# Kernel optimization log

Hardware: AMD Instinct MI355X
Metric: run time of the kernel (lower is better)

## Reference

```python
import jax, jax.numpy as jnp
import numpy as np

N_NODES = 60000
IN_CH = 128
HID = 32
ACT_DIM = 6
N_EDGES = 600000


def setup_inputs() -> dict:
    key = jax.random.key(0)
    ks = jax.random.split(key, 10)
    state = jax.random.normal(ks[0], (N_NODES, IN_CH), dtype=jnp.float32)
    edge_index = jax.random.randint(ks[1], (2, N_EDGES), 0, N_NODES, dtype=jnp.int64)
    s_g = 1.0 / np.sqrt(IN_CH)
    s_h = 1.0 / np.sqrt(HID)
    Wg = jax.random.uniform(ks[2], (IN_CH, IN_CH), jnp.float32, -s_g, s_g)
    bg = jax.random.uniform(ks[3], (IN_CH,), jnp.float32, -s_g, s_g)
    W1 = jax.random.uniform(ks[4], (IN_CH, HID), jnp.float32, -s_g, s_g)
    b1 = jax.random.uniform(ks[5], (HID,), jnp.float32, -s_g, s_g)
    W2 = jax.random.uniform(ks[6], (HID, HID), jnp.float32, -s_h, s_h)
    b2 = jax.random.uniform(ks[7], (HID,), jnp.float32, -s_h, s_h)
    W3 = jax.random.uniform(ks[8], (HID, 1), jnp.float32, -s_h, s_h)
    b3 = jax.random.uniform(ks[9], (1,), jnp.float32, -s_h, s_h)
    return {"state": state, "Wg": Wg, "bg": bg, "W1": W1, "b1": b1,
            "W2": W2, "b2": b2, "W3": W3, "b3": b3, "edge_index": edge_index}


def reference(state, Wg, bg, W1, b1, W2, b2, W3, b3, edge_index):
    N = state.shape[0]
    # GCNConv: add self-loops, symmetric degree normalization
    loop = jnp.arange(N, dtype=edge_index.dtype)
    src = jnp.concatenate([edge_index[0], loop])
    dst = jnp.concatenate([edge_index[1], loop])
    deg = jax.ops.segment_sum(jnp.ones_like(dst, dtype=state.dtype), dst, num_segments=N)
    dinv = jax.lax.rsqrt(deg)  # deg >= 1 thanks to self-loops
    norm = dinv[src] * dinv[dst]  # [E+N]
    h = state @ Wg  # [N, C]
    agg = jax.ops.segment_sum(h[src] * norm[:, None], dst, num_segments=N) + bg
    out = jax.nn.relu(agg)
    x = (out + state).reshape(-1, ACT_DIM, IN_CH)  # [B, 6, C]
    x = jax.nn.leaky_relu(x @ W1 + b1)
    x = jax.nn.leaky_relu(x @ W2 + b2)
    conc = jax.nn.softplus(x @ W3 + b3)[..., 0]  # [B, 6]
    # deterministic, mode==0
    action = conc / (conc.sum() + 1e-20)
    return action
```

## Files before the change

### kernel.cpp

```cpp
#include <hip/hip_runtime.h>
#include <hip/hip_bf16.h>
#include <math.h>

#define N_NODES 60000
#define IN_CH   128
#define HID     32
#define N_EDGES 600000
#define CAP     48

#define WS_CNT    0
#define WS_SUM    60000
#define WS_BUCKET 60008
#define WS_HS     2940032
#define WS_X      10620032

typedef float  v4f __attribute__((ext_vector_type(4)));
typedef short  v8s __attribute__((ext_vector_type(8)));

static __device__ inline short f2bf(float f) {
    __hip_bfloat16 h = __float2bfloat16(f);
    union { __hip_bfloat16 h; short s; } u; u.h = h; return u.s;
}

__global__ void k_hist(const int* __restrict__ eidx, int* __restrict__ cnt,
                       int* __restrict__ bucket) {
    int i = blockIdx.x * blockDim.x + threadIdx.x;
    if (i >= N_EDGES) return;
    int s = eidx[i];
    int d = eidx[N_EDGES + i];
    int slot = atomicAdd(&cnt[d], 1);
    if (slot < CAP) bucket[d * CAP + slot] = s;
}

__launch_bounds__(256)
__global__ void k_gemm(const float* __restrict__ state, const float* __restrict__ Wg,
                       const int* __restrict__ cnt, unsigned short* __restrict__ hs) {
    __shared__ __align__(16) short Bs[128 * 136];
    const int t = threadIdx.x;
    for (int idx = t; idx < 128 * 128; idx += 256) {
        int k = idx >> 7, n = idx & 127;
        Bs[n * 136 + k] = f2bf(Wg[idx]);
    }
    __syncthreads();

    const int w = t >> 6, lane = t & 63;
    const int quad = lane >> 4, m = lane & 15;
    const int rowBase = blockIdx.x * 64;
    int arow = rowBase + w * 16 + m;
    if (arow > N_NODES - 1) arow = N_NODES - 1;

    v8s a[4];
    const float4* sp = (const float4*)(state + (size_t)arow * 128);
#pragma unroll
    for (int q = 0; q < 4; ++q) {
        float4 v0 = sp[q * 8 + quad * 2];
        float4 v1 = sp[q * 8 + quad * 2 + 1];
        v8s af;
        af[0] = f2bf(v0.x); af[1] = f2bf(v0.y); af[2] = f2bf(v0.z); af[3] = f2bf(v0.w);
        af[4] = f2bf(v1.x); af[5] = f2bf(v1.y); af[6] = f2bf(v1.z); af[7] = f2bf(v1.w);
        a[q] = af;
    }

    v4f acc[8];
#pragma unroll
    for (int tt = 0; tt < 8; ++tt) acc[tt] = (v4f)0.f;

#pragma unroll
    for (int tt = 0; tt < 8; ++tt) {
        const short* bp = &Bs[(tt * 16 + m) * 136];
#pragma unroll
        for (int q = 0; q < 4; ++q) {
            v8s b = *(const v8s*)(bp + q * 32 + quad * 8);
            acc[tt] = __builtin_amdgcn_mfma_f32_16x16x32_bf16(a[q], b, acc[tt], 0, 0, 0);
        }
    }

    float dinv[4];
#pragma unroll
    for (int r = 0; r < 4; ++r) {
        int rr = rowBase + w * 16 + quad * 4 + r;
        dinv[r] = (rr < N_NODES) ? rsqrtf((float)cnt[rr] + 1.0f) : 0.f;
    }
#pragma unroll
    for (int tt = 0; tt < 8; ++tt) {
#pragma unroll
        for (int r = 0; r < 4; ++r) {
            int rr = rowBase + w * 16 + quad * 4 + r;
            if (rr < N_NODES)
                hs[(size_t)rr * 128 + tt * 16 + m] = (unsigned short)f2bf(acc[tt][r] * dinv[r]);
        }
    }
}

__launch_bounds__(256)
__global__ void k_gather(const unsigned short* __restrict__ hs, const float* __restrict__ state,
                         const int* __restrict__ cnt, const int* __restrict__ bucket,
                         const float* __restrict__ bg, float* __restrict__ x) {
    const int wave = threadIdx.x >> 6, lane = threadIdx.x & 63;
    const int row = blockIdx.x * 4 + wave;
    if (row >= N_NODES) return;
    const int ci = cnt[row];
    const float dinv = rsqrtf((float)ci + 1.0f);
    const int nb = ci < CAP ? ci : CAP;

    int slot = (lane < nb) ? bucket[row * CAP + lane] : 0;

    const unsigned int* hp = (const unsigned int*)hs;
    float ax, ay;
    {
        unsigned int u = hp[row * 64 + lane];
        ax = __uint_as_float(u << 16);
        ay = __uint_as_float(u & 0xffff0000u);
    }
    int s = 0;
    for (; s + 8 <= nb; s += 8) {
        unsigned int u0 = hp[__shfl(slot, s + 0, 64) * 64 + lane];
        unsigned int u1 = hp[__shfl(slot, s + 1, 64) * 64 + lane];
        unsigned int u2 = hp[__shfl(slot, s + 2, 64) * 64 + lane];
        unsigned int u3 = hp[__shfl(slot, s + 3, 64) * 64 + lane];
        unsigned int u4 = hp[__shfl(slot, s + 4, 64) * 64 + lane];
        unsigned int u5 = hp[__shfl(slot, s + 5, 64) * 64 + lane];
        unsigned int u6 = hp[__shfl(slot, s + 6, 64) * 64 + lane];
        unsigned int u7 = hp[__shfl(slot, s + 7, 64) * 64 + lane];
        ax += __uint_as_float(u0 << 16) + __uint_as_float(u1 << 16)
            + __uint_as_float(u2 << 16) + __uint_as_float(u3 << 16)
            + __uint_as_float(u4 << 16) + __uint_as_float(u5 << 16)
            + __uint_as_float(u6 << 16) + __uint_as_float(u7 << 16);
        ay += __uint_as_float(u0 & 0xffff0000u) + __uint_as_float(u1 & 0xffff0000u)
            + __uint_as_float(u2 & 0xffff0000u) + __uint_as_float(u3 & 0xffff0000u)
            + __uint_as_float(u4 & 0xffff0000u) + __uint_as_float(u5 & 0xffff0000u)
            + __uint_as_float(u6 & 0xffff0000u) + __uint_as_float(u7 & 0xffff0000u);
    }
    for (; s + 4 <= nb; s += 4) {
        unsigned int u0 = hp[__shfl(slot, s + 0, 64) * 64 + lane];
        unsigned int u1 = hp[__shfl(slot, s + 1, 64) * 64 + lane];
        unsigned int u2 = hp[__shfl(slot, s + 2, 64) * 64 + lane];
        unsigned int u3 = hp[__shfl(slot, s + 3, 64) * 64 + lane];
        ax += __uint_as_float(u0 << 16) + __uint_as_float(u1 << 16)
            + __uint_as_float(u2 << 16) + __uint_as_float(u3 << 16);
        ay += __uint_as_float(u0 & 0xffff0000u) + __uint_as_float(u1 & 0xffff0000u)
            + __uint_as_float(u2 & 0xffff0000u) + __uint_as_float(u3 & 0xffff0000u);
    }
    for (; s < nb; ++s) {
        unsigned int u = hp[__shfl(slot, s, 64) * 64 + lane];
        ax += __uint_as_float(u << 16);
        ay += __uint_as_float(u & 0xffff0000u);
    }
    float2 bgv = ((const float2*)bg)[lane];
    float2 st  = ((const float2*)state)[row * 64 + lane];
    float2 o;
    o.x = fmaxf(fmaf(dinv, ax, bgv.x), 0.f) + st.x;
    o.y = fmaxf(fmaf(dinv, ay, bgv.y), 0.f) + st.y;
    ((float2*)x)[row * 64 + lane] = o;
}

__launch_bounds__(256)
__global__ void k_mlp(const float* __restrict__ x,
                      const float* __restrict__ W1, const float* __restrict__ b1,
                      const float* __restrict__ W2, const float* __restrict__ b2,
                      const float* __restrict__ W3, const float* __restrict__ b3,
                      float* __restrict__ out, float* __restrict__ sum) {
    __shared__ float4 W1s[128 * 8];
    __shared__ float4 W2s[32 * 8];
    __shared__ float  W3s[32];
    __shared__ float  wred[4];
    const int t = threadIdx.x;
#pragma unroll
    for (int i = 0; i < 4; ++i) W1s[t + 256 * i] = ((const float4*)W1)[t + 256 * i];
    W2s[t] = ((const float4*)W2)[t];
    if (t < 32) W3s[t] = W3[t];
    __syncthreads();

    const int r = blockIdx.x * 256 + t;
    float sp = 0.f;
    if (r < N_NODES) {
        float h1[32];
#pragma unroll
        for (int j = 0; j < 32; ++j) h1[j] = b1[j];
        const float4* xr = (const float4*)(x + (size_t)r * 128);
#pragma unroll 4
        for (int k4 = 0; k4 < 32; ++k4) {
            float4 xv = xr[k4];
            float xa[4] = {xv.x, xv.y, xv.z, xv.w};
#pragma unroll
            for (int kk = 0; kk < 4; ++kk) {
                float xk = xa[kk];
#pragma unroll
                for (int j4 = 0; j4 < 8; ++j4) {
                    float4 w = W1s[(k4 * 4 + kk) * 8 + j4];
                    h1[j4 * 4 + 0] = fmaf(xk, w.x, h1[j4 * 4 + 0]);
                    h1[j4 * 4 + 1] = fmaf(xk, w.y, h1[j4 * 4 + 1]);
                    h1[j4 * 4 + 2] = fmaf(xk, w.z, h1[j4 * 4 + 2]);
                    h1[j4 * 4 + 3] = fmaf(xk, w.w, h1[j4 * 4 + 3]);
                }
            }
        }
        float z1[32];
#pragma unroll
        for (int j = 0; j < 32; ++j) z1[j] = h1[j] > 0.f ? h1[j] : 0.01f * h1[j];
        float h2[32];
#pragma unroll
        for (int j = 0; j < 32; ++j) h2[j] = b2[j];
#pragma unroll
        for (int k = 0; k < 32; ++k) {
            float zk = z1[k];
#pragma unroll
            for (int j4 = 0; j4 < 8; ++j4) {
                float4 w = W2s[k * 8 + j4];
                h2[j4 * 4 + 0] = fmaf(zk, w.x, h2[j4 * 4 + 0]);
                h2[j4 * 4 + 1] = fmaf(zk, w.y, h2[j4 * 4 + 1]);
                h2[j4 * 4 + 2] = fmaf(zk, w.z, h2[j4 * 4 + 2]);
                h2[j4 * 4 + 3] = fmaf(zk, w.w, h2[j4 * 4 + 3]);
            }
        }
        float a3 = b3[0];
#pragma unroll
        for (int j = 0; j < 32; ++j) {
            float z2 = h2[j] > 0.f ? h2[j] : 0.01f * h2[j];
            a3 = fmaf(z2, W3s[j], a3);
        }
        sp = fmaxf(a3, 0.f) + log1pf(expf(-fabsf(a3)));
        out[r] = sp;
    }
    float p = sp;
#pragma unroll
    for (int off = 32; off >= 1; off >>= 1) p += __shfl_xor(p, off, 64);
    if ((t & 63) == 0) wred[t >> 6] = p;
    __syncthreads();
    if (t == 0) atomicAdd(sum, (wred[0] + wred[1]) + (wred[2] + wred[3]));
}

__global__ void k_norm(const float* __restrict__ sum, float* __restrict__ out) {
    int i = blockIdx.x * blockDim.x + threadIdx.x;
    if (i < N_NODES) out[i] = out[i] / (*sum + 1e-20f);
}

extern "C" void kernel_launch(void* const* d_in, const int* in_sizes, int n_in,
                              void* d_out, int out_size, void* d_ws, size_t ws_size,
                              hipStream_t stream) {
    const float* state = (const float*)d_in[0];
    const float* Wg    = (const float*)d_in[1];
    const float* bg    = (const float*)d_in[2];
    const float* W1    = (const float*)d_in[3];
    const float* b1    = (const float*)d_in[4];
    const float* W2    = (const float*)d_in[5];
    const float* b2    = (const float*)d_in[6];
    const float* W3    = (const float*)d_in[7];
    const float* b3    = (const float*)d_in[8];
    const int*   eidx  = (const int*)d_in[9];
    float* out = (float*)d_out;

    int*   wi = (int*)d_ws;
    float* wf = (float*)d_ws;
    int*   cnt    = wi + WS_CNT;
    float* sum    = wf + WS_SUM;
    int*   bucket = wi + WS_BUCKET;
    unsigned short* hs = (unsigned short*)(wf + WS_HS);
    float* x      = wf + WS_X;

    hipMemsetAsync(cnt, 0, 60001 * sizeof(int), stream);
    k_hist<<<(N_EDGES + 255) / 256, 256, 0, stream>>>(eidx, cnt, bucket);
    k_gemm<<<(N_NODES + 63) / 64, 256, 0, stream>>>(state, Wg, cnt, hs);
    k_gather<<<(N_NODES + 3) / 4, 256, 0, stream>>>(hs, state, cnt, bucket, bg, x);
    k_mlp<<<(N_NODES + 255) / 256, 256, 0, stream>>>(x, W1, b1, W2, b2, W3, b3, out, sum);
    k_norm<<<(N_NODES + 255) / 256, 256, 0, stream>>>(sum, out);
}
```

Before: 190.4 us.

## Fuse gather and MLP into persistent kernel, pre-convert Wg, shrink bucket to u16

Merges the neighbor gather and the per-node MLP into one persistent grid-stride kernel. Each wave computes a node's aggregated features into shared memory and evaluates the small MLP cooperatively with lane-parallel dot products and shuffles, so the fp32 x intermediate is never written to or read from global memory. Wg is converted to transposed bf16 once in the histogram kernel rather than in every GEMM block, and bucket indices are stored as 16-bit values. Node ids up to 60000 fit in an unsigned short, but the MLP now runs per row with heavy shuffle and LDS traffic, which may reduce throughput.

After: 240.1 us. 1.26x slower.

```diff
diff --git a/kernel.cpp b/kernel.cpp
--- a/kernel.cpp
+++ b/kernel.cpp
@@ -10,9 +10,9 @@
 
 #define WS_CNT    0
 #define WS_SUM    60000
-#define WS_BUCKET 60008
-#define WS_HS     2940032
-#define WS_X      10620032
+#define WS_WGT    60004
+#define WS_BUCKET 68200
+#define WS_HS     1508200
 
 typedef float  v4f __attribute__((ext_vector_type(4)));
 typedef short  v8s __attribute__((ext_vector_type(8)));
@@ -23,23 +23,30 @@
 }
 
 __global__ void k_hist(const int* __restrict__ eidx, int* __restrict__ cnt,
-                       int* __restrict__ bucket) {
+                       unsigned short* __restrict__ bucket,
+                       const float* __restrict__ Wg, unsigned short* __restrict__ wgt) {
     int i = blockIdx.x * blockDim.x + threadIdx.x;
-    if (i >= N_EDGES) return;
-    int s = eidx[i];
-    int d = eidx[N_EDGES + i];
-    int slot = atomicAdd(&cnt[d], 1);
-    if (slot < CAP) bucket[d * CAP + slot] = s;
+    if (i < N_EDGES) {
+        int s = eidx[i];
+        int d = eidx[N_EDGES + i];
+        int slot = atomicAdd(&cnt[d], 1);
+        if (slot < CAP) bucket[d * CAP + slot] = (unsigned short)s;
+    }
+    if (i < IN_CH * IN_CH) {
+        int k = i >> 7, n = i & 127;
+        wgt[n * 128 + k] = (unsigned short)f2bf(Wg[i]);
+    }
 }
 
 __launch_bounds__(256)
-__global__ void k_gemm(const float* __restrict__ state, const float* __restrict__ Wg,
+__global__ void k_gemm(const float* __restrict__ state, const unsigned short* __restrict__ wgt,
                        const int* __restrict__ cnt, unsigned short* __restrict__ hs) {
     __shared__ __align__(16) short Bs[128 * 136];
     const int t = threadIdx.x;
-    for (int idx = t; idx < 128 * 128; idx += 256) {
-        int k = idx >> 7, n = idx & 127;
-        Bs[n * 136 + k] = f2bf(Wg[idx]);
+    for (int i = t; i < 2048; i += 256) {
+        int n = i >> 4, kc = i & 15;
+        v8s v = *(const v8s*)(wgt + n * 128 + kc * 8);
+        *(v8s*)&Bs[n * 136 + kc * 8] = v;
     }
     __syncthreads();
 
@@ -64,7 +71,6 @@
     v4f acc[8];
 #pragma unroll
     for (int tt = 0; tt < 8; ++tt) acc[tt] = (v4f)0.f;
-
 #pragma unroll
     for (int tt = 0; tt < 8; ++tt) {
         const short* bp = &Bs[(tt * 16 + m) * 136];
@@ -93,139 +99,112 @@
 }
 
 __launch_bounds__(256)
-__global__ void k_gather(const unsigned short* __restrict__ hs, const float* __restrict__ state,
-                         const int* __restrict__ cnt, const int* __restrict__ bucket,
-                         const float* __restrict__ bg, float* __restrict__ x) {
-    const int wave = threadIdx.x >> 6, lane = threadIdx.x & 63;
-    const int row = blockIdx.x * 4 + wave;
-    if (row >= N_NODES) return;
-    const int ci = cnt[row];
-    const float dinv = rsqrtf((float)ci + 1.0f);
-    const int nb = ci < CAP ? ci : CAP;
-
-    int slot = (lane < nb) ? bucket[row * CAP + lane] : 0;
-
+__global__ void k_gather_mlp(const unsigned short* __restrict__ hs, const float* __restrict__ state,
+                             const int* __restrict__ cnt, const unsigned short* __restrict__ bucket,
+                             const float* __restrict__ bg,
+                             const float* __restrict__ W1, const float* __restrict__ b1,
+                             const float* __restrict__ W2, const float* __restrict__ b2,
+                             const float* __restrict__ W3, const float* __restrict__ b3,
+                             float* __restrict__ out, float* __restrict__ sum) {
+    __shared__ float W1s[128 * 32];
+    __shared__ float W2s[32 * 32];
+    __shared__ float xs[4][128];
+    __shared__ float wred[4];
+    const int t = threadIdx.x;
+#pragma unroll
+    for (int i = 0; i < 4; ++i)
+        ((float4*)W1s)[t + 256 * i] = ((const float4*)W1)[t + 256 * i];
+    ((float4*)W2s)[t] = ((const float4*)W2)[t];
+    __syncthreads();
+
+    const int wave = t >> 6, lane = t & 63;
+    const int j = lane & 31;
+    const int khalf = (lane >> 5) * 64;
+    const int k2 = (lane >> 5) * 16;
+    const float2 bgv = ((const float2*)bg)[lane];
+    const float b1r = b1[j];
+    const float b2r = b2[j];
+    const float w3r = (lane < 32) ? W3[j] : 0.f;
+    const float b3v = b3[0];
     const unsigned int* hp = (const unsigned int*)hs;
-    float ax, ay;
-    {
-        unsigned int u = hp[row * 64 + lane];
-        ax = __uint_as_float(u << 16);
-        ay = __uint_as_float(u & 0xffff0000u);
-    }
-    int s = 0;
-    for (; s + 8 <= nb; s += 8) {
-        unsigned int u0 = hp[__shfl(slot, s + 0, 64) * 64 + lane];
-        unsigned int u1 = hp[__shfl(slot, s + 1, 64) * 64 + lane];
-        unsigned int u2 = hp[__shfl(slot, s + 2, 64) * 64 + lane];
-        unsigned int u3 = hp[__shfl(slot, s + 3, 64) * 64 + lane];
-        unsigned int u4 = hp[__shfl(slot, s + 4, 64) * 64 + lane];
-        unsigned int u5 = hp[__shfl(slot, s + 5, 64) * 64 + lane];
-        unsigned int u6 = hp[__shfl(slot, s + 6, 64) * 64 + lane];
-        unsigned int u7 = hp[__shfl(slot, s + 7, 64) * 64 + lane];
-        ax += __uint_as_float(u0 << 16) + __uint_as_float(u1 << 16)
-            + __uint_as_float(u2 << 16) + __uint_as_float(u3 << 16)
-            + __uint_as_float(u4 << 16) + __uint_as_float(u5 << 16)
-            + __uint_as_float(u6 << 16) + __uint_as_float(u7 << 16);
-        ay += __uint_as_float(u0 & 0xffff0000u) + __uint_as_float(u1 & 0xffff0000u)
-            + __uint_as_float(u2 & 0xffff0000u) + __uint_as_float(u3 & 0xffff0000u)
-            + __uint_as_float(u4 & 0xffff0000u) + __uint_as_float(u5 & 0xffff0000u)
-            + __uint_as_float(u6 & 0xffff0000u) + __uint_as_float(u7 & 0xffff0000u);
-    }
-    for (; s + 4 <= nb; s += 4) {
-        unsigned int u0 = hp[__shfl(slot, s + 0, 64) * 64 + lane];
-        unsigned int u1 = hp[__shfl(slot, s + 1, 64) * 64 + lane];
-        unsigned int u2 = hp[__shfl(slot, s + 2, 64) * 64 + lane];
-        unsigned int u3 = hp[__shfl(slot, s + 3, 64) * 64 + lane];
-        ax += __uint_as_float(u0 << 16) + __uint_as_float(u1 << 16)
-            + __uint_as_float(u2 << 16) + __uint_as_float(u3 << 16);
-        ay += __uint_as_float(u0 & 0xffff0000u) + __uint_as_float(u1 & 0xffff0000u)
-            + __uint_as_float(u2 & 0xffff0000u) + __uint_as_float(u3 & 0xffff0000u);
-    }
-    for (; s < nb; ++s) {
-        unsigned int u = hp[__shfl(slot, s, 64) * 64 + lane];
-        ax += __uint_as_float(u << 16);
-        ay += __uint_as_float(u & 0xffff0000u);
-    }
-    float2 bgv = ((const float2*)bg)[lane];
-    float2 st  = ((const float2*)state)[row * 64 + lane];
-    float2 o;
-    o.x = fmaxf(fmaf(dinv, ax, bgv.x), 0.f) + st.x;
-    o.y = fmaxf(fmaf(dinv, ay, bgv.y), 0.f) + st.y;
-    ((float2*)x)[row * 64 + lane] = o;
-}
-
-__launch_bounds__(256)
-__global__ void k_mlp(const float* __restrict__ x,
-                      const float* __restrict__ W1, const float* __restrict__ b1,
-                      const float* __restrict__ W2, const float* __restrict__ b2,
-                      const float* __restrict__ W3, const float* __restrict__ b3,
-                      float* __restrict__ out, float* __restrict__ sum) {
-    __shared__ float4 W1s[128 * 8];
-    __shared__ float4 W2s[32 * 8];
-    __shared__ float  W3s[32];
-    __shared__ float  wred[4];
-    const int t = threadIdx.x;
-#pragma unroll
-    for (int i = 0; i < 4; ++i) W1s[t + 256 * i] = ((const float4*)W1)[t + 256 * i];
-    W2s[t] = ((const float4*)W2)[t];
-    if (t < 32) W3s[t] = W3[t];
-    __syncthreads();
-
-    const int r = blockIdx.x * 256 + t;
-    float sp = 0.f;
-    if (r < N_NODES) {
-        float h1[32];
-#pragma unroll
-        for (int j = 0; j < 32; ++j) h1[j] = b1[j];
-        const float4* xr = (const float4*)(x + (size_t)r * 128);
-#pragma unroll 4
-        for (int k4 = 0; k4 < 32; ++k4) {
-            float4 xv = xr[k4];
-            float xa[4] = {xv.x, xv.y, xv.z, xv.w};
-#pragma unroll
-            for (int kk = 0; kk < 4; ++kk) {
-                float xk = xa[kk];
-#pragma unroll
-                for (int j4 = 0; j4 < 8; ++j4) {
-                    float4 w = W1s[(k4 * 4 + kk) * 8 + j4];
-                    h1[j4 * 4 + 0] = fmaf(xk, w.x, h1[j4 * 4 + 0]);
-                    h1[j4 * 4 + 1] = fmaf(xk, w.y, h1[j4 * 4 + 1]);
-                    h1[j4 * 4 + 2] = fmaf(xk, w.z, h1[j4 * 4 + 2]);
-                    h1[j4 * 4 + 3] = fmaf(xk, w.w, h1[j4 * 4 + 3]);
-                }
-            }
-        }
-        float z1[32];
-#pragma unroll
-        for (int j = 0; j < 32; ++j) z1[j] = h1[j] > 0.f ? h1[j] : 0.01f * h1[j];
-        float h2[32];
-#pragma unroll
-        for (int j = 0; j < 32; ++j) h2[j] = b2[j];
-#pragma unroll
-        for (int k = 0; k < 32; ++k) {
-            float zk = z1[k];
-#pragma unroll
-            for (int j4 = 0; j4 < 8; ++j4) {
-                float4 w = W2s[k * 8 + j4];
-                h2[j4 * 4 + 0] = fmaf(zk, w.x, h2[j4 * 4 + 0]);
-                h2[j4 * 4 + 1] = fmaf(zk, w.y, h2[j4 * 4 + 1]);
-                h2[j4 * 4 + 2] = fmaf(zk, w.z, h2[j4 * 4 + 2]);
-                h2[j4 * 4 + 3] = fmaf(zk, w.w, h2[j4 * 4 + 3]);
-            }
-        }
-        float a3 = b3[0];
-#pragma unroll
-        for (int j = 0; j < 32; ++j) {
-            float z2 = h2[j] > 0.f ? h2[j] : 0.01f * h2[j];
-            a3 = fmaf(z2, W3s[j], a3);
-        }
-        sp = fmaxf(a3, 0.f) + log1pf(expf(-fabsf(a3)));
-        out[r] = sp;
-    }
-    float p = sp;
-#pragma unroll
-    for (int off = 32; off >= 1; off >>= 1) p += __shfl_xor(p, off, 64);
-    if ((t & 63) == 0) wred[t >> 6] = p;
+
+    float csum = 0.f;
+    for (int row = blockIdx.x * 4 + wave; row < N_NODES; row += gridDim.x * 4) {
+        const int ci = cnt[row];
+        const float dinv = rsqrtf((float)ci + 1.0f);
+        const int nb = ci < CAP ? ci : CAP;
+        int slot = (lane < nb) ? (int)bucket[row * CAP + lane] : 0;
+
+        float ax, ay;
+        {
+            unsigned int u = hp[row * 64 + lane];
+            ax = __uint_as_float(u << 16);
+            ay = __uint_as_float(u & 0xffff0000u);
+        }
+        int s = 0;
+        for (; s + 8 <= nb; s += 8) {
+            unsigned int u0 = hp[__shfl(slot, s + 0, 64) * 64 + lane];
+            unsigned int u1 = hp[__shfl(slot, s + 1, 64) * 64 + lane];
+            unsigned int u2 = hp[__shfl(slot, s + 2, 64) * 64 + lane];
+            unsigned int u3 = hp[__shfl(slot, s + 3, 64) * 64 + lane];
+            unsigned int u4 = hp[__shfl(slot, s + 4, 64) * 64 + lane];
+            unsigned int u5 = hp[__shfl(slot, s + 5, 64) * 64 + lane];
+            unsigned int u6 = hp[__shfl(slot, s + 6, 64) * 64 + lane];
+            unsigned int u7 = hp[__shfl(slot, s + 7, 64) * 64 + lane];
+            ax += __uint_as_float(u0 << 16) + __uint_as_float(u1 << 16)
+                + __uint_as_float(u2 << 16) + __uint_as_float(u3 << 16)
+                + __uint_as_float(u4 << 16) + __uint_as_float(u5 << 16)
+                + __uint_as_float(u6 << 16) + __uint_as_float(u7 << 16);
+            ay += __uint_as_float(u0 & 0xffff0000u) + __uint_as_float(u1 & 0xffff0000u)
+                + __uint_as_float(u2 & 0xffff0000u) + __uint_as_float(u3 & 0xffff0000u)
+                + __uint_as_float(u4 & 0xffff0000u) + __uint_as_float(u5 & 0xffff0000u)
+                + __uint_as_float(u6 & 0xffff0000u) + __uint_as_float(u7 & 0xffff0000u);
+        }
+        for (; s + 4 <= nb; s += 4) {
+            unsigned int u0 = hp[__shfl(slot, s + 0, 64) * 64 + lane];
+            unsigned int u1 = hp[__shfl(slot, s + 1, 64) * 64 + lane];
+            unsigned int u2 = hp[__shfl(slot, s + 2, 64) * 64 + lane];
+            unsigned int u3 = hp[__shfl(slot, s + 3, 64) * 64 + lane];
+            ax += __uint_as_float(u0 << 16) + __uint_as_float(u1 << 16)
+                + __uint_as_float(u2 << 16) + __uint_as_float(u3 << 16);
+            ay += __uint_as_float(u0 & 0xffff0000u) + __uint_as_float(u1 & 0xffff0000u)
+                + __uint_as_float(u2 & 0xffff0000u) + __uint_as_float(u3 & 0xffff0000u);
+        }
+        for (; s < nb; ++s) {
+            unsigned int u = hp[__shfl(slot, s, 64) * 64 + lane];
+            ax += __uint_as_float(u << 16);
+            ay += __uint_as_float(u & 0xffff0000u);
+        }
+        float2 st = ((const float2*)state)[row * 64 + lane];
+        float x0 = fmaxf(fmaf(dinv, ax, bgv.x), 0.f) + st.x;
+        float x1 = fmaxf(fmaf(dinv, ay, bgv.y), 0.f) + st.y;
+        xs[wave][2 * lane]     = x0;
+        xs[wave][2 * lane + 1] = x1;
+
+        float a1 = 0.f;
+#pragma unroll
+        for (int kk = 0; kk < 64; ++kk)
+            a1 = fmaf(xs[wave][khalf + kk], W1s[(khalf + kk) * 32 + j], a1);
+        float y1 = a1 + __shfl_xor(a1, 32, 64) + b1r;
+        float z1 = y1 > 0.f ? y1 : 0.01f * y1;
+
+        float a2 = 0.f;
+#pragma unroll
+        for (int kk = 0; kk < 16; ++kk) {
+            float zk = __shfl(z1, k2 + kk, 64);
+            a2 = fmaf(zk, W2s[(k2 + kk) * 32 + j], a2);
+        }
+        float y2 = a2 + __shfl_xor(a2, 32, 64) + b2r;
+        float z2 = y2 > 0.f ? y2 : 0.01f * y2;
+
+        float p = z2 * w3r;
+#pragma unroll
+        for (int off = 32; off >= 1; off >>= 1) p += __shfl_xor(p, off, 64);
+        float v3 = p + b3v;
+        float sp = fmaxf(v3, 0.f) + log1pf(expf(-fabsf(v3)));
+        if (lane == 0) { out[row] = sp; csum += sp; }
+    }
+    if (lane == 0) wred[wave] = csum;
     __syncthreads();
     if (t == 0) atomicAdd(sum, (wred[0] + wred[1]) + (wred[2] + wred[3]));
 }
@@ -252,16 +231,16 @@
 
     int*   wi = (int*)d_ws;
     float* wf = (float*)d_ws;
-    int*   cnt    = wi + WS_CNT;
-    float* sum    = wf + WS_SUM;
-    int*   bucket = wi + WS_BUCKET;
-    unsigned short* hs = (unsigned short*)(wf + WS_HS);
-    float* x      = wf + WS_X;
+    int*            cnt    = wi + WS_CNT;
+    float*          sum    = wf + WS_SUM;
+    unsigned short* wgt    = (unsigned short*)(wf + WS_WGT);
+    unsigned short* bucket = (unsigned short*)(wf + WS_BUCKET);
+    unsigned short* hs     = (unsigned short*)(wf + WS_HS);
 
     hipMemsetAsync(cnt, 0, 60001 * sizeof(int), stream);
-    k_hist<<<(N_EDGES + 255) / 256, 256, 0, stream>>>(eidx, cnt, bucket);
-    k_gemm<<<(N_NODES + 63) / 64, 256, 0, stream>>>(state, Wg, cnt, hs);
-    k_gather<<<(N_NODES + 3) / 4, 256, 0, stream>>>(hs, state, cnt, bucket, bg, x);
-    k_mlp<<<(N_NODES + 255) / 256, 256, 0, stream>>>(x, W1, b1, W2, b2, W3, b3, out, sum);
+    k_hist<<<(N_EDGES + 255) / 256, 256, 0, stream>>>(eidx, cnt, bucket, Wg, wgt);
+    k_gemm<<<(N_NODES + 63) / 64, 256, 0, stream>>>(state, wgt, cnt, hs);
+    k_gather_mlp<<<1792, 256, 0, stream>>>(hs, state, cnt, bucket, bg,
+                                           W1, b1, W2, b2, W3, b3, out, sum);
     k_norm<<<(N_NODES + 255) / 256, 256, 0, stream>>>(sum, out);
 }
```

## Store x and buckets in 16-bit, pre-convert Wg to bf16 once

Applied to the files above, without the earlier changes.

The intermediate x between gather and MLP is now packed as bf16 pairs instead of fp32, halving that write and read. Bucket source indices are stored as 16-bit values, which is valid only because N_NODES is under 65536. The Wg to bf16 transpose now runs once in the histogram kernel, so each GEMM block loads pre-converted weights with vector loads instead of converting 128x128 floats itself. The cost is lower precision on the MLP input and a 16-bit index limit.

Measured after the change: 193.8 us. About the same (+1.8%).

```diff
diff --git a/kernel.cpp b/kernel.cpp
--- a/kernel.cpp
+++ b/kernel.cpp
@@ -10,9 +10,10 @@
 
 #define WS_CNT    0
 #define WS_SUM    60000
-#define WS_BUCKET 60008
-#define WS_HS     2940032
-#define WS_X      10620032
+#define WS_WGT    60004
+#define WS_BUCKET 68200
+#define WS_HS     1508200
+#define WS_X      5348200
 
 typedef float  v4f __attribute__((ext_vector_type(4)));
 typedef short  v8s __attribute__((ext_vector_type(8)));
@@ -21,25 +22,36 @@
     __hip_bfloat16 h = __float2bfloat16(f);
     union { __hip_bfloat16 h; short s; } u; u.h = h; return u.s;
 }
+static __device__ inline unsigned int pack2bf(float a, float b) {
+    return ((unsigned int)(unsigned short)f2bf(a)) |
+           (((unsigned int)(unsigned short)f2bf(b)) << 16);
+}
 
 __global__ void k_hist(const int* __restrict__ eidx, int* __restrict__ cnt,
-                       int* __restrict__ bucket) {
+                       unsigned short* __restrict__ bucket,
+                       const float* __restrict__ Wg, unsigned short* __restrict__ wgt) {
     int i = blockIdx.x * blockDim.x + threadIdx.x;
-    if (i >= N_EDGES) return;
-    int s = eidx[i];
-    int d = eidx[N_EDGES + i];
-    int slot = atomicAdd(&cnt[d], 1);
-    if (slot < CAP) bucket[d * CAP + slot] = s;
+    if (i < N_EDGES) {
+        int s = eidx[i];
+        int d = eidx[N_EDGES + i];
+        int slot = atomicAdd(&cnt[d], 1);
+        if (slot < CAP) bucket[d * CAP + slot] = (unsigned short)s;
+    }
+    if (i < IN_CH * IN_CH) {
+        int k = i >> 7, n = i & 127;
+        wgt[n * 128 + k] = (unsigned short)f2bf(Wg[i]);
+    }
 }
 
 __launch_bounds__(256)
-__global__ void k_gemm(const float* __restrict__ state, const float* __restrict__ Wg,
+__global__ void k_gemm(const float* __restrict__ state, const unsigned short* __restrict__ wgt,
                        const int* __restrict__ cnt, unsigned short* __restrict__ hs) {
     __shared__ __align__(16) short Bs[128 * 136];
     const int t = threadIdx.x;
-    for (int idx = t; idx < 128 * 128; idx += 256) {
-        int k = idx >> 7, n = idx & 127;
-        Bs[n * 136 + k] = f2bf(Wg[idx]);
+    for (int i = t; i < 2048; i += 256) {
+        int n = i >> 4, kc = i & 15;
+        v8s v = *(const v8s*)(wgt + n * 128 + kc * 8);
+        *(v8s*)&Bs[n * 136 + kc * 8] = v;
     }
     __syncthreads();
 
@@ -64,7 +76,6 @@
     v4f acc[8];
 #pragma unroll
     for (int tt = 0; tt < 8; ++tt) acc[tt] = (v4f)0.f;
-
 #pragma unroll
     for (int tt = 0; tt < 8; ++tt) {
         const short* bp = &Bs[(tt * 16 + m) * 136];
@@ -94,16 +105,15 @@
 
 __launch_bounds__(256)
 __global__ void k_gather(const unsigned short* __restrict__ hs, const float* __restrict__ state,
-                         const int* __restrict__ cnt, const int* __restrict__ bucket,
-                         const float* __restrict__ bg, float* __restrict__ x) {
+                         const int* __restrict__ cnt, const unsigned short* __restrict__ bucket,
+                         const float* __restrict__ bg, unsigned int* __restrict__ x) {
     const int wave = threadIdx.x >> 6, lane = threadIdx.x & 63;
     const int row = blockIdx.x * 4 + wave;
     if (row >= N_NODES) return;
     const int ci = cnt[row];
     const float dinv = rsqrtf((float)ci + 1.0f);
     const int nb = ci < CAP ? ci : CAP;
-
-    int slot = (lane < nb) ? bucket[row * CAP + lane] : 0;
+    int slot = (lane < nb) ? (int)bucket[row * CAP + lane] : 0;
 
     const unsigned int* hp = (const unsigned int*)hs;
     float ax, ay;
@@ -148,14 +158,13 @@
     }
     float2 bgv = ((const float2*)bg)[lane];
     float2 st  = ((const float2*)state)[row * 64 + lane];
-    float2 o;
-    o.x = fmaxf(fmaf(dinv, ax, bgv.x), 0.f) + st.x;
-    o.y = fmaxf(fmaf(dinv, ay, bgv.y), 0.f) + st.y;
-    ((float2*)x)[row * 64 + lane] = o;
+    float x0 = fmaxf(fmaf(dinv, ax, bgv.x), 0.f) + st.x;
+    float x1 = fmaxf(fmaf(dinv, ay, bgv.y), 0.f) + st.y;
+    x[row * 64 + lane] = pack2bf(x0, x1);
 }
 
 __launch_bounds__(256)
-__global__ void k_mlp(const float* __restrict__ x,
+__global__ void k_mlp(const unsigned int* __restrict__ x,
                       const float* __restrict__ W1, const float* __restrict__ b1,
                       const float* __restrict__ W2, const float* __restrict__ b2,
                       const float* __restrict__ W3, const float* __restrict__ b3,
@@ -177,21 +186,31 @@
         float h1[32];
 #pragma unroll
         for (int j = 0; j < 32; ++j) h1[j] = b1[j];
-        const float4* xr = (const float4*)(x + (size_t)r * 128);
+        const uint4* xr = (const uint4*)(x + (size_t)r * 64);
 #pragma unroll 4
-        for (int k4 = 0; k4 < 32; ++k4) {
-            float4 xv = xr[k4];
-            float xa[4] = {xv.x, xv.y, xv.z, xv.w};
-#pragma unroll
-            for (int kk = 0; kk < 4; ++kk) {
-                float xk = xa[kk];
+        for (int c4 = 0; c4 < 16; ++c4) {
+            uint4 uv = xr[c4];
+            unsigned int ua[4] = {uv.x, uv.y, uv.z, uv.w};
+#pragma unroll
+            for (int d = 0; d < 4; ++d) {
+                float xe = __uint_as_float(ua[d] << 16);
+                float xo = __uint_as_float(ua[d] & 0xffff0000u);
+                int k = c4 * 8 + d * 2;
 #pragma unroll
                 for (int j4 = 0; j4 < 8; ++j4) {
-                    float4 w = W1s[(k4 * 4 + kk) * 8 + j4];
-                    h1[j4 * 4 + 0] = fmaf(xk, w.x, h1[j4 * 4 + 0]);
-                    h1[j4 * 4 + 1] = fmaf(xk, w.y, h1[j4 * 4 + 1]);
-                    h1[j4 * 4 + 2] = fmaf(xk, w.z, h1[j4 * 4 + 2]);
-                    h1[j4 * 4 + 3] = fmaf(xk, w.w, h1[j4 * 4 + 3]);
+                    float4 we = W1s[k * 8 + j4];
+                    h1[j4 * 4 + 0] = fmaf(xe, we.x, h1[j4 * 4 + 0]);
+                    h1[j4 * 4 + 1] = fmaf(xe, we.y, h1[j4 * 4 + 1]);
+                    h1[j4 * 4 + 2] = fmaf(xe, we.z, h1[j4 * 4 + 2]);
+                    h1[j4 * 4 + 3] = fmaf(xe, we.w, h1[j4 * 4 + 3]);
+                }
+#pragma unroll
+                for (int j4 = 0; j4 < 8; ++j4) {
+                    float4 wo = W1s[(k + 1) * 8 + j4];
+                    h1[j4 * 4 + 0] = fmaf(xo, wo.x, h1[j4 * 4 + 0]);
+                    h1[j4 * 4 + 1] = fmaf(xo, wo.y, h1[j4 * 4 + 1]);
+                    h1[j4 * 4 + 2] = fmaf(xo, wo.z, h1[j4 * 4 + 2]);
+                    h1[j4 * 4 + 3] = fmaf(xo, wo.w, h1[j4 * 4 + 3]);
                 }
             }
         }
@@ -252,15 +271,16 @@
 
     int*   wi = (int*)d_ws;
     float* wf = (float*)d_ws;
-    int*   cnt    = wi + WS_CNT;
-    float* sum    = wf + WS_SUM;
-    int*   bucket = wi + WS_BUCKET;
-    unsigned short* hs = (unsigned short*)(wf + WS_HS);
-    float* x      = wf + WS_X;
+    int*            cnt    = wi + WS_CNT;
+    float*          sum    = wf + WS_SUM;
+    unsigned short* wgt    = (unsigned short*)(wf + WS_WGT);
+    unsigned short* bucket = (unsigned short*)(wf + WS_BUCKET);
+    unsigned short* hs     = (unsigned short*)(wf + WS_HS);
+    unsigned int*   x      = (unsigned int*)(wf + WS_X);
 
     hipMemsetAsync(cnt, 0, 60001 * sizeof(int), stream);
-    k_hist<<<(N_EDGES + 255) / 256, 256, 0, stream>>>(eidx, cnt, bucket);
-    k_gemm<<<(N_NODES + 63) / 64, 256, 0, stream>>>(state, Wg, cnt, hs);
+    k_hist<<<(N_EDGES + 255) / 256, 256, 0, stream>>>(eidx, cnt, bucket, Wg, wgt);
+    k_gemm<<<(N_NODES + 63) / 64, 256, 0, stream>>>(state, wgt, cnt, hs);
     k_gather<<<(N_NODES + 3) / 4, 256, 0, stream>>>(hs, state, cnt, bucket, bg, x);
     k_mlp<<<(N_NODES + 255) / 256, 256, 0, stream>>>(x, W1, b1, W2, b2, W3, b3, out, sum);
     k_norm<<<(N_NODES + 255) / 256, 256, 0, stream>>>(sum, out);
```
